# Performance work log

Hardware: AMD Instinct MI355X
Metric: run time of the kernel (lower is better)

The kernel has to match this reference:

```python
import jax, jax.numpy as jnp
import numpy as np

DIM = 1024
HEADS = 8
HEAD_DIM = DIM // HEADS
D_STATE = 256
BATCH = 8192
DT_MIN = 1e-3
DT_MAX = 1e-1
EPS = 1e-4  # RMSNorm eps


def setup_inputs() -> dict:
    key = jax.random.key(0)
    ks = jax.random.split(key, 8)
    x_t = jax.random.normal(ks[0], (BATCH, DIM), dtype=jnp.float32)
    state_re = jax.random.normal(ks[1], (BATCH, HEADS, D_STATE), dtype=jnp.float32)
    state_im = jax.random.normal(ks[2], (BATCH, HEADS, D_STATE), dtype=jnp.float32)
    # parameters (match torch init)
    norm_weight = jnp.ones((DIM,), dtype=jnp.float32)
    A_re_log = jnp.full((HEADS, D_STATE), float(np.log(0.5)), dtype=jnp.float32)
    n = jnp.arange(1, D_STATE + 1, dtype=jnp.float32)
    A_im = jnp.broadcast_to(float(np.pi) * n, (HEADS, D_STATE)).astype(jnp.float32)
    b_scale = 1.0 / float(np.sqrt(HEAD_DIM))
    c_scale = 1.0 / float(np.sqrt(D_STATE))
    B_re = jax.random.normal(ks[3], (HEADS, D_STATE, HEAD_DIM), dtype=jnp.float32) * b_scale
    B_im = jax.random.normal(ks[4], (HEADS, D_STATE, HEAD_DIM), dtype=jnp.float32) * b_scale
    C_re = jax.random.normal(ks[5], (HEADS, HEAD_DIM, D_STATE), dtype=jnp.float32) * c_scale
    C_im = jax.random.normal(ks[6], (HEADS, HEAD_DIM, D_STATE), dtype=jnp.float32) * c_scale
    D = jnp.ones((DIM,), dtype=jnp.float32)
    # log_dt: inverse-softplus of log-uniform dt in [dt_min, dt_max]
    u = jax.random.uniform(ks[7], (HEADS, D_STATE), dtype=jnp.float32)
    dt = jnp.exp(u * (np.log(DT_MAX) - np.log(DT_MIN)) + np.log(DT_MIN))
    dt = jnp.maximum(dt, 1e-4)
    log_dt = dt + jnp.log(-jnp.expm1(-dt))
    return dict(x_t=x_t, state_re=state_re, state_im=state_im,
                norm_weight=norm_weight, A_re_log=A_re_log, A_im=A_im,
                B_re=B_re, B_im=B_im, C_re=C_re, C_im=C_im, D=D, log_dt=log_dt)


def reference(x_t, state_re, state_im, norm_weight, A_re_log, A_im,
              B_re, B_im, C_re, C_im, D, log_dt):
    batch = x_t.shape[0]
    # RMSNorm (eps=1e-4, elementwise affine)
    ms = jnp.mean(jnp.square(x_t), axis=-1, keepdims=True)
    x = x_t * jax.lax.rsqrt(ms + EPS) * norm_weight
    x_h = x.reshape(batch, HEADS, HEAD_DIM)  # (B,H,P)
    # discretize
    A = jax.lax.complex(-jnp.exp(A_re_log), A_im)            # (H,N)
    dt = jax.nn.softplus(log_dt)                              # (H,N)
    A_bar = jnp.exp(dt.astype(A.dtype) * A)                   # (H,N) complex
    B = jax.lax.complex(B_re, B_im)                           # (H,N,P)
    C = jax.lax.complex(C_re, C_im)                           # (H,P,N)
    B_bar = ((A_bar - 1.0) / A)[..., None] * B                # (H,N,P)
    # recurrent step
    state = jax.lax.complex(state_re, state_im)               # (B,H,N)
    Bx = jnp.einsum('hnp,bhp->bhn', B_bar, x_h.astype(B_bar.dtype))
    new_state = A_bar[None] * state + Bx                      # (B,H,N)
    Ch = jnp.einsum('hpn,bhn->bhp', C, new_state)             # (B,H,P)
    D_h = D.reshape(HEADS, HEAD_DIM)[None]                    # (1,H,P)
    y_h = 2.0 * Ch.real + D_h * x_h
    out = x_t + y_h.reshape(batch, DIM)
    return out, new_state.real, new_state.imag
```

## Files before the change

kernel.cpp:

```cpp
#include <hip/hip_runtime.h>

#define BATCH 8192
#define DIM 1024
#define HEADS 8
#define HEAD_DIM 128
#define DSTATE 256

typedef __attribute__((ext_vector_type(8))) short short8v;
typedef __attribute__((ext_vector_type(4))) float f32x4;
typedef __attribute__((ext_vector_type(4))) unsigned short ushort4v;
typedef __attribute__((ext_vector_type(4))) unsigned int uint4v;

__device__ __forceinline__ unsigned short f2bf(float x) {
  unsigned int u = __builtin_bit_cast(unsigned int, x);
  unsigned int r = u + 0x7FFFu + ((u >> 16) & 1u);
  return (unsigned short)(r >> 16);
}
__device__ __forceinline__ float bf2f(unsigned short h) {
  unsigned int u = ((unsigned int)h) << 16;
  return __builtin_bit_cast(float, u);
}

__device__ __forceinline__ void stage16f(const float* g, float* l) {
  __builtin_amdgcn_global_load_lds(
      (const __attribute__((address_space(1))) unsigned int*)g,
      (__attribute__((address_space(3))) unsigned int*)l, 16, 0, 0);
}
__device__ __forceinline__ void stage4f(const float* g, float* l) {
  __builtin_amdgcn_global_load_lds(
      (const __attribute__((address_space(1))) unsigned int*)g,
      (__attribute__((address_space(3))) unsigned int*)l, 4, 0, 0);
}

#define BARRIER() do { \
  asm volatile("s_waitcnt lgkmcnt(0)" ::: "memory"); \
  __builtin_amdgcn_s_barrier(); \
  asm volatile("" ::: "memory"); } while (0)


__global__ __launch_bounds__(256) void prep(
    const float* __restrict__ logdt, const float* __restrict__ arelog,
    const float* __restrict__ aim,
    const float* __restrict__ Bre, const float* __restrict__ Bim,
    const float* __restrict__ Cre, const float* __restrict__ Cim,
    const float* __restrict__ xtg, const float* __restrict__ normw,
    unsigned short* __restrict__ w1re, unsigned short* __restrict__ w1im,
    unsigned short* __restrict__ w2re, unsigned short* __restrict__ w2mi,
    float* __restrict__ abr, float* __restrict__ abi,
    float* __restrict__ scale) {
  const int blk = blockIdx.x;
  if (blk < 1024) {
    const int i = blk * 256 + threadIdx.x;
    const int p = i & 127, s = (i >> 7) & 255, h = i >> 15;
    const int kk = s >> 4, u = s & 15;
    const int n = ((kk >> 1) << 5) + ((u >> 2) & 3) * 8 + (kk & 1) * 4 + (u & 3);
    const int hn = h * 256 + n;
    const float ld = logdt[hn];
    const float dt = log1pf(expf(ld));
    const float Ar = -expf(arelog[hn]);
    const float Ai = aim[hn];
    const float e = expf(dt * Ar), th = dt * Ai;
    const float Abr = e * cosf(th), Abi = e * sinf(th);
    if (p == 0) { abr[h * 256 + s] = Abr; abi[h * 256 + s] = Abi; }
    const float den = Ar * Ar + Ai * Ai;
    const float br_ = Abr - 1.0f;
    const float cr = (br_ * Ar + Abi * Ai) / den;
    const float ci = (Abi * Ar - br_ * Ai) / den;
    const int src = hn * 128 + p;
    const float wb = normw[h * 128 + p];
    const float bre = Bre[src], bim = Bim[src];
    w1re[i] = f2bf((cr * bre - ci * bim) * wb);
    w1im[i] = f2bf((cr * bim + ci * bre) * wb);
  } else if (blk < 2048) {
    const int i = (blk - 1024) * 256 + threadIdx.x;
    w2re[i] = f2bf(Cre[i]);
    w2mi[i] = f2bf(-Cim[i]);
  } else {
    const int wid = threadIdx.x >> 6, lane = threadIdx.x & 63;
    const int row = (blk - 2048) * 4 + wid;
    const float* xr = xtg + (size_t)row * DIM;
    float ssq = 0.f;
    #pragma unroll
    for (int c = 0; c < 4; ++c) {
      const f32x4 v = *(const f32x4*)(xr + c * 256 + lane * 4);
      ssq += v[0]*v[0] + v[1]*v[1] + v[2]*v[2] + v[3]*v[3];
    }
    #pragma unroll
    for (int m = 1; m < 64; m <<= 1) ssq += __shfl_xor(ssq, m, 64);
    if (lane == 0) scale[row] = rsqrtf(ssq * (1.0f / DIM) + 1e-4f);
  }
}

__global__ __launch_bounds__(512, 2) void s5_main(
    const unsigned short* __restrict__ w1re, const unsigned short* __restrict__ w1im,
    const unsigned short* __restrict__ w2re, const unsigned short* __restrict__ w2mi,
    const float* __restrict__ abrp, const float* __restrict__ abip,
    const float* __restrict__ scale,
    const float* __restrict__ sre, const float* __restrict__ sim,
    const float* __restrict__ xt, const float* __restrict__ dvec,
    const float* __restrict__ normw,
    float* __restrict__ out, float* __restrict__ nsre, float* __restrict__ nsim) {
  __shared__ float Sb[3][2][16][256];
  __shared__ float xtl[3][16][128];
  __shared__ unsigned short pf[2][8][64][8];
  __shared__ float scL[3][64];
  const int tid = threadIdx.x;
  const int w = tid >> 6, lane = tid & 63;
  const int g = lane >> 4, bl = lane & 15;
  const int h = blockIdx.x & 7;
  const int blkrow = (blockIdx.x >> 3) * 256;

  short8v w1r[2][4], w1i[2][4];
  #pragma unroll
  for (int t = 0; t < 2; ++t) {
    const int kk = 2 * w + t;
    const unsigned short* pr = w1re + ((size_t)(h * DSTATE + kk * 16 + bl)) * HEAD_DIM + g * 8;
    const unsigned short* pi = w1im + ((size_t)(h * DSTATE + kk * 16 + bl)) * HEAD_DIM + g * 8;
    #pragma unroll
    for (int ks = 0; ks < 4; ++ks) {
      w1r[t][ks] = *(const short8v*)(pr + ks * 32);
      w1i[t][ks] = *(const short8v*)(pi + ks * 32);
    }
  }
  short8v w2r[8], w2i[8];
  {
    const unsigned short* qr = w2re + ((size_t)(h * HEAD_DIM + w * 16 + bl)) * DSTATE + g * 8;
    const unsigned short* qi = w2mi + ((size_t)(h * HEAD_DIM + w * 16 + bl)) * DSTATE + g * 8;
    #pragma unroll
    for (int j = 0; j < 8; ++j) {
      w2r[j] = *(const short8v*)(qr + j * 32);
      w2i[j] = *(const short8v*)(qi + j * 32);
    }
  }
  f32x4 Arh[2], Aih[2];
  #pragma unroll
  for (int t = 0; t < 2; ++t) {
    Arh[t] = *(const f32x4*)(abrp + h * DSTATE + (2 * w + t) * 16 + g * 4);
    Aih[t] = *(const f32x4*)(abip + h * DSTATE + (2 * w + t) * 16 + g * 4);
  }
  f32x4 d4;
  {
    const int col = h * HEAD_DIM + w * 16 + g * 4;
    const f32x4 dv = *(const f32x4*)(dvec + col);
    const f32x4 nv = *(const f32x4*)(normw + col);
    #pragma unroll
    for (int r = 0; r < 4; ++r) d4[r] = dv[r] * nv[r];
  }

  auto STAGE = [&](int t, int b3) {
    const int gr0 = blkrow + t * 16;
    #pragma unroll
    for (int i = 0; i < 2; ++i) {
      const int row = 2 * w + i;
      const size_t rb = ((size_t)(gr0 + row) * HEADS + h) * DSTATE;
      const int soff = (lane ^ (row & 7)) * 4;
      stage16f(sre + rb + soff, &Sb[b3][0][row][0]);
      stage16f(sim + rb + soff, &Sb[b3][1][row][0]);
    }
    {
      const int row = 2 * w + (lane >> 5);
      const int soff = ((lane & 31) ^ (row & 7)) * 4;
      const float* src = xt + (size_t)(gr0 + row) * DIM + h * HEAD_DIM + soff;
      stage16f(src, &xtl[b3][2 * w][0]);
    }
    stage4f(scale + gr0 + (lane & 15), &scL[b3][0]);
  };

  STAGE(0, 0);
  STAGE(1, 1);

  for (int t = 0; t < 16; ++t) {
    const int bcur = t % 3;
    if (t < 2) { asm volatile("s_waitcnt vmcnt(6)"  ::: "memory"); }
    else       { asm volatile("s_waitcnt vmcnt(10)" ::: "memory"); }
    BARRIER();

    if (t + 2 < 16) STAGE(t + 2, (t + 2) % 3);

    const float scl = scL[bcur][bl];
    short8v xf[4];
    #pragma unroll
    for (int ks = 0; ks < 4; ++ks) {
      const f32x4 x0 = *(const f32x4*)&xtl[bcur][bl][(((ks * 8 + 2 * g)     ^ (bl & 7)) << 2)];
      const f32x4 x1 = *(const f32x4*)&xtl[bcur][bl][(((ks * 8 + 2 * g + 1) ^ (bl & 7)) << 2)];
      uint4v uv;
      uv[0] = (unsigned)f2bf(x0[0] * scl) | ((unsigned)f2bf(x0[1] * scl) << 16);
      uv[1] = (unsigned)f2bf(x0[2] * scl) | ((unsigned)f2bf(x0[3] * scl) << 16);
      uv[2] = (unsigned)f2bf(x1[0] * scl) | ((unsigned)f2bf(x1[1] * scl) << 16);
      uv[3] = (unsigned)f2bf(x1[2] * scl) | ((unsigned)f2bf(x1[3] * scl) << 16);
      xf[ks] = __builtin_bit_cast(short8v, uv);
    }

    unsigned pr0 = 0, pr1 = 0, pi0 = 0, pi1 = 0;
    #pragma unroll
    for (int tt = 0; tt < 2; ++tt) {
      f32x4 dr = {0.f,0.f,0.f,0.f};
      f32x4 di = {0.f,0.f,0.f,0.f};
      #pragma unroll
      for (int ks = 0; ks < 4; ++ks)
        dr = __builtin_amdgcn_mfma_f32_16x16x32_bf16(w1r[tt][ks], xf[ks], dr, 0, 0, 0);
      #pragma unroll
      for (int ks = 0; ks < 4; ++ks)
        di = __builtin_amdgcn_mfma_f32_16x16x32_bf16(w1i[tt][ks], xf[ks], di, 0, 0, 0);
      const int c = (((8 * w + 2 * g + tt) ^ (bl & 7)) << 2);
      const f32x4 s_r = *(const f32x4*)&Sb[bcur][0][bl][c];
      const f32x4 s_i = *(const f32x4*)&Sb[bcur][1][bl][c];
      f32x4 nr, ni;
      #pragma unroll
      for (int r = 0; r < 4; ++r) {
        nr[r] = fmaf(Arh[tt][r], s_r[r], fmaf(-Aih[tt][r], s_i[r], dr[r]));
        ni[r] = fmaf(Arh[tt][r], s_i[r], fmaf(Aih[tt][r], s_r[r], di[r]));
      }
      *(f32x4*)&Sb[bcur][0][bl][c] = nr;
      *(f32x4*)&Sb[bcur][1][bl][c] = ni;
      unsigned lo  = (unsigned)f2bf(nr[0]) | ((unsigned)f2bf(nr[1]) << 16);
      unsigned hi  = (unsigned)f2bf(nr[2]) | ((unsigned)f2bf(nr[3]) << 16);
      unsigned lo2 = (unsigned)f2bf(ni[0]) | ((unsigned)f2bf(ni[1]) << 16);
      unsigned hi2 = (unsigned)f2bf(ni[2]) | ((unsigned)f2bf(ni[3]) << 16);
      if (tt == 0) { pr0 = lo; pr1 = hi; pi0 = lo2; pi1 = hi2; }
      else {
        uint4v urv; urv[0] = pr0; urv[1] = pr1; urv[2] = lo;  urv[3] = hi;
        uint4v uiv; uiv[0] = pi0; uiv[1] = pi1; uiv[2] = lo2; uiv[3] = hi2;
        *(short8v*)&pf[0][w][lane][0] = __builtin_bit_cast(short8v, urv);
        *(short8v*)&pf[1][w][lane][0] = __builtin_bit_cast(short8v, uiv);
      }
    }
    BARRIER();

    #pragma unroll
    for (int i = 0; i < 2; ++i) {
      const int row = 2 * w + i;
      const size_t rb = ((size_t)(blkrow + t * 16 + row) * HEADS + h) * DSTATE;
      const int gc = (lane ^ (row & 7)) * 4;
      const f32x4 vr = *(const f32x4*)&Sb[bcur][0][row][lane * 4];
      const f32x4 vi = *(const f32x4*)&Sb[bcur][1][row][lane * 4];
      *(f32x4*)(nsre + rb + gc) = vr;
      *(f32x4*)(nsim + rb + gc) = vi;
    }

    f32x4 a2 = {0.f,0.f,0.f,0.f};
    #pragma unroll
    for (int j = 0; j < 8; ++j) {
      const short8v pbr = *(const short8v*)&pf[0][j][lane][0];
      const short8v pbi = *(const short8v*)&pf[1][j][lane][0];
      a2 = __builtin_amdgcn_mfma_f32_16x16x32_bf16(w2r[j], pbr, a2, 0, 0, 0);
      a2 = __builtin_amdgcn_mfma_f32_16x16x32_bf16(w2i[j], pbi, a2, 0, 0, 0);
    }

    {
      const int col = h * HEAD_DIM + w * 16 + g * 4;
      const size_t o = (size_t)(blkrow + t * 16 + bl) * DIM + col;
      const f32x4 xt4 = *(const f32x4*)&xtl[bcur][bl][(((4 * w + g) ^ (bl & 7)) << 2)];
      f32x4 ro;
      #pragma unroll
      for (int r = 0; r < 4; ++r)
        ro[r] = xt4[r] * (1.0f + d4[r] * scl) + 2.0f * a2[r];
      *(f32x4*)(out + o) = ro;
    }
  }
}

extern "C" void kernel_launch(void* const* d_in, const int* in_sizes, int n_in,
                              void* d_out, int out_size, void* d_ws, size_t ws_size,
                              hipStream_t stream) {
  const float* x_t      = (const float*)d_in[0];
  const float* state_re = (const float*)d_in[1];
  const float* state_im = (const float*)d_in[2];
  const float* norm_w   = (const float*)d_in[3];
  const float* A_re_log = (const float*)d_in[4];
  const float* A_im     = (const float*)d_in[5];
  const float* B_re     = (const float*)d_in[6];
  const float* B_im     = (const float*)d_in[7];
  const float* C_re     = (const float*)d_in[8];
  const float* C_im     = (const float*)d_in[9];
  const float* Dv       = (const float*)d_in[10];
  const float* log_dt   = (const float*)d_in[11];

  float* out   = (float*)d_out;
  float* ns_re = out + (size_t)BATCH * DIM;
  float* ns_im = ns_re + (size_t)BATCH * HEADS * DSTATE;

  char* ws = (char*)d_ws;
  unsigned short* w1re = (unsigned short*)ws;
  unsigned short* w1im = w1re + 262144;
  unsigned short* w2re = w1im + 262144;
  unsigned short* w2mi = w2re + 262144;
  float* abr   = (float*)(ws + 4 * 524288);
  float* abi   = abr + 2048;
  float* scale = abi + 2048;

  prep<<<4096, 256, 0, stream>>>(log_dt, A_re_log, A_im, B_re, B_im, C_re, C_im,
                                 x_t, norm_w, w1re, w1im, w2re, w2mi,
                                 abr, abi, scale);
  s5_main<<<256, 512, 0, stream>>>(w1re, w1im, w2re, w2mi, abr, abi, scale,
                                   state_re, state_im, x_t, Dv, norm_w,
                                   out, ns_re, ns_im);
}
```

Baseline: 92.30 us.

## Software-pipeline S5 phases, stage bf16 x_t, and drop the pf LDS buffer

The prep kernel now also writes a bf16 copy of x_t, and the main kernel stages that copy instead of fp32 x_t. The per-tile loop is restructured so the output phase of tile t-1 overlaps the state-update phase of tile t. This uses a 4-deep state ring and one barrier per iteration instead of two. The second MFMA reads the updated state straight from Sb instead of a separate packed pf buffer, and the output and state stores are made nontemporal. The risk is accuracy: the residual x_t added to out is now read back from bf16, and the prep kernel has extra writes.

```diff
diff --git a/kernel.cpp b/kernel.cpp
--- a/kernel.cpp
+++ b/kernel.cpp
@@ -26,7 +26,7 @@
       (const __attribute__((address_space(1))) unsigned int*)g,
       (__attribute__((address_space(3))) unsigned int*)l, 16, 0, 0);
 }
-__device__ __forceinline__ void stage4f(const float* g, float* l) {
+__device__ __forceinline__ void stage4u(const unsigned short* g, unsigned short* l) {
   __builtin_amdgcn_global_load_lds(
       (const __attribute__((address_space(1))) unsigned int*)g,
       (__attribute__((address_space(3))) unsigned int*)l, 4, 0, 0);
@@ -47,7 +47,7 @@
     unsigned short* __restrict__ w1re, unsigned short* __restrict__ w1im,
     unsigned short* __restrict__ w2re, unsigned short* __restrict__ w2mi,
     float* __restrict__ abr, float* __restrict__ abi,
-    float* __restrict__ scale) {
+    float* __restrict__ scale, unsigned short* __restrict__ xtb) {
   const int blk = blockIdx.x;
   if (blk < 1024) {
     const int i = blk * 256 + threadIdx.x;
@@ -79,11 +79,15 @@
     const int wid = threadIdx.x >> 6, lane = threadIdx.x & 63;
     const int row = (blk - 2048) * 4 + wid;
     const float* xr = xtg + (size_t)row * DIM;
+    unsigned short* xo = xtb + (size_t)row * DIM;
     float ssq = 0.f;
     #pragma unroll
     for (int c = 0; c < 4; ++c) {
       const f32x4 v = *(const f32x4*)(xr + c * 256 + lane * 4);
       ssq += v[0]*v[0] + v[1]*v[1] + v[2]*v[2] + v[3]*v[3];
+      ushort4v o;
+      o[0] = f2bf(v[0]); o[1] = f2bf(v[1]); o[2] = f2bf(v[2]); o[3] = f2bf(v[3]);
+      *(ushort4v*)(xo + c * 256 + lane * 4) = o;
     }
     #pragma unroll
     for (int m = 1; m < 64; m <<= 1) ssq += __shfl_xor(ssq, m, 64);
@@ -95,15 +99,13 @@
     const unsigned short* __restrict__ w1re, const unsigned short* __restrict__ w1im,
     const unsigned short* __restrict__ w2re, const unsigned short* __restrict__ w2mi,
     const float* __restrict__ abrp, const float* __restrict__ abip,
-    const float* __restrict__ scale,
+    const float* __restrict__ scale, const unsigned short* __restrict__ xtb,
     const float* __restrict__ sre, const float* __restrict__ sim,
-    const float* __restrict__ xt, const float* __restrict__ dvec,
-    const float* __restrict__ normw,
+    const float* __restrict__ dvec, const float* __restrict__ normw,
     float* __restrict__ out, float* __restrict__ nsre, float* __restrict__ nsim) {
-  __shared__ float Sb[3][2][16][256];
-  __shared__ float xtl[3][16][128];
-  __shared__ unsigned short pf[2][8][64][8];
-  __shared__ float scL[3][64];
+  __shared__ float Sb[4][2][16][256];
+  __shared__ unsigned short xbL[4][16][128];
+  __shared__ float scL[256];
   const int tid = threadIdx.x;
   const int w = tid >> 6, lane = tid & 63;
   const int g = lane >> 4, bl = lane & 15;
@@ -147,51 +149,42 @@
     for (int r = 0; r < 4; ++r) d4[r] = dv[r] * nv[r];
   }
 
-  auto STAGE = [&](int t, int b3) {
+  auto STAGE = [&](int t, int b) {
     const int gr0 = blkrow + t * 16;
     #pragma unroll
     for (int i = 0; i < 2; ++i) {
       const int row = 2 * w + i;
       const size_t rb = ((size_t)(gr0 + row) * HEADS + h) * DSTATE;
       const int soff = (lane ^ (row & 7)) * 4;
-      stage16f(sre + rb + soff, &Sb[b3][0][row][0]);
-      stage16f(sim + rb + soff, &Sb[b3][1][row][0]);
-    }
-    {
-      const int row = 2 * w + (lane >> 5);
-      const int soff = ((lane & 31) ^ (row & 7)) * 4;
-      const float* src = xt + (size_t)(gr0 + row) * DIM + h * HEAD_DIM + soff;
-      stage16f(src, &xtl[b3][2 * w][0]);
-    }
-    stage4f(scale + gr0 + (lane & 15), &scL[b3][0]);
+      stage16f(sre + rb + soff, &Sb[b][0][row][0]);
+      stage16f(sim + rb + soff, &Sb[b][1][row][0]);
+    }
+    #pragma unroll
+    for (int i = 0; i < 2; ++i) {
+      const int row = 2 * w + i;
+      const unsigned short* src = xtb + (size_t)(gr0 + row) * DIM + h * HEAD_DIM
+          + (((lane >> 2) ^ (row & 7)) << 3) + ((lane & 3) << 1);
+      stage4u(src, &xbL[b][row][0]);
+    }
   };
 
-  STAGE(0, 0);
-  STAGE(1, 1);
-
-  for (int t = 0; t < 16; ++t) {
-    const int bcur = t % 3;
-    if (t < 2) { asm volatile("s_waitcnt vmcnt(6)"  ::: "memory"); }
-    else       { asm volatile("s_waitcnt vmcnt(10)" ::: "memory"); }
-    BARRIER();
-
-    if (t + 2 < 16) STAGE(t + 2, (t + 2) % 3);
-
-    const float scl = scL[bcur][bl];
+  auto PHASE1 = [&](int t) {
+    const int b = t & 3;
+    const float scl = scL[t * 16 + bl];
     short8v xf[4];
     #pragma unroll
     for (int ks = 0; ks < 4; ++ks) {
-      const f32x4 x0 = *(const f32x4*)&xtl[bcur][bl][(((ks * 8 + 2 * g)     ^ (bl & 7)) << 2)];
-      const f32x4 x1 = *(const f32x4*)&xtl[bcur][bl][(((ks * 8 + 2 * g + 1) ^ (bl & 7)) << 2)];
-      uint4v uv;
-      uv[0] = (unsigned)f2bf(x0[0] * scl) | ((unsigned)f2bf(x0[1] * scl) << 16);
-      uv[1] = (unsigned)f2bf(x0[2] * scl) | ((unsigned)f2bf(x0[3] * scl) << 16);
-      uv[2] = (unsigned)f2bf(x1[0] * scl) | ((unsigned)f2bf(x1[1] * scl) << 16);
-      uv[3] = (unsigned)f2bf(x1[2] * scl) | ((unsigned)f2bf(x1[3] * scl) << 16);
-      xf[ks] = __builtin_bit_cast(short8v, uv);
-    }
-
-    unsigned pr0 = 0, pr1 = 0, pi0 = 0, pi1 = 0;
+      const int ch = (ks * 4 + g) ^ (bl & 7);
+      uint4v u = *(const uint4v*)&xbL[b][bl][ch * 8];
+      uint4v o;
+      #pragma unroll
+      for (int q = 0; q < 4; ++q) {
+        const float lo = bf2f((unsigned short)(u[q] & 0xffffu)) * scl;
+        const float hi = bf2f((unsigned short)(u[q] >> 16)) * scl;
+        o[q] = (unsigned)f2bf(lo) | ((unsigned)f2bf(hi) << 16);
+      }
+      xf[ks] = __builtin_bit_cast(short8v, o);
+    }
     #pragma unroll
     for (int tt = 0; tt < 2; ++tt) {
       f32x4 dr = {0.f,0.f,0.f,0.f};
@@ -203,61 +196,86 @@
       for (int ks = 0; ks < 4; ++ks)
         di = __builtin_amdgcn_mfma_f32_16x16x32_bf16(w1i[tt][ks], xf[ks], di, 0, 0, 0);
       const int c = (((8 * w + 2 * g + tt) ^ (bl & 7)) << 2);
-      const f32x4 s_r = *(const f32x4*)&Sb[bcur][0][bl][c];
-      const f32x4 s_i = *(const f32x4*)&Sb[bcur][1][bl][c];
+      const f32x4 s_r = *(const f32x4*)&Sb[b][0][bl][c];
+      const f32x4 s_i = *(const f32x4*)&Sb[b][1][bl][c];
       f32x4 nr, ni;
       #pragma unroll
       for (int r = 0; r < 4; ++r) {
         nr[r] = fmaf(Arh[tt][r], s_r[r], fmaf(-Aih[tt][r], s_i[r], dr[r]));
         ni[r] = fmaf(Arh[tt][r], s_i[r], fmaf(Aih[tt][r], s_r[r], di[r]));
       }
-      *(f32x4*)&Sb[bcur][0][bl][c] = nr;
-      *(f32x4*)&Sb[bcur][1][bl][c] = ni;
-      unsigned lo  = (unsigned)f2bf(nr[0]) | ((unsigned)f2bf(nr[1]) << 16);
-      unsigned hi  = (unsigned)f2bf(nr[2]) | ((unsigned)f2bf(nr[3]) << 16);
-      unsigned lo2 = (unsigned)f2bf(ni[0]) | ((unsigned)f2bf(ni[1]) << 16);
-      unsigned hi2 = (unsigned)f2bf(ni[2]) | ((unsigned)f2bf(ni[3]) << 16);
-      if (tt == 0) { pr0 = lo; pr1 = hi; pi0 = lo2; pi1 = hi2; }
-      else {
-        uint4v urv; urv[0] = pr0; urv[1] = pr1; urv[2] = lo;  urv[3] = hi;
-        uint4v uiv; uiv[0] = pi0; uiv[1] = pi1; uiv[2] = lo2; uiv[3] = hi2;
-        *(short8v*)&pf[0][w][lane][0] = __builtin_bit_cast(short8v, urv);
-        *(short8v*)&pf[1][w][lane][0] = __builtin_bit_cast(short8v, uiv);
-      }
-    }
-    BARRIER();
-
+      *(f32x4*)&Sb[b][0][bl][c] = nr;
+      *(f32x4*)&Sb[b][1][bl][c] = ni;
+    }
+  };
+
+  auto PHASE2 = [&](int t) {
+    const int b = t & 3;
     #pragma unroll
     for (int i = 0; i < 2; ++i) {
       const int row = 2 * w + i;
       const size_t rb = ((size_t)(blkrow + t * 16 + row) * HEADS + h) * DSTATE;
       const int gc = (lane ^ (row & 7)) * 4;
-      const f32x4 vr = *(const f32x4*)&Sb[bcur][0][row][lane * 4];
-      const f32x4 vi = *(const f32x4*)&Sb[bcur][1][row][lane * 4];
-      *(f32x4*)(nsre + rb + gc) = vr;
-      *(f32x4*)(nsim + rb + gc) = vi;
-    }
-
+      const f32x4 vr = *(const f32x4*)&Sb[b][0][row][lane * 4];
+      const f32x4 vi = *(const f32x4*)&Sb[b][1][row][lane * 4];
+      __builtin_nontemporal_store(vr, (f32x4*)(nsre + rb + gc));
+      __builtin_nontemporal_store(vi, (f32x4*)(nsim + rb + gc));
+    }
     f32x4 a2 = {0.f,0.f,0.f,0.f};
     #pragma unroll
     for (int j = 0; j < 8; ++j) {
-      const short8v pbr = *(const short8v*)&pf[0][j][lane][0];
-      const short8v pbi = *(const short8v*)&pf[1][j][lane][0];
+      const int c0 = (((8 * j + 2 * g)     ^ (bl & 7)) << 2);
+      const int c1 = (((8 * j + 2 * g + 1) ^ (bl & 7)) << 2);
+      const f32x4 r0 = *(const f32x4*)&Sb[b][0][bl][c0];
+      const f32x4 r1 = *(const f32x4*)&Sb[b][0][bl][c1];
+      const f32x4 i0 = *(const f32x4*)&Sb[b][1][bl][c0];
+      const f32x4 i1 = *(const f32x4*)&Sb[b][1][bl][c1];
+      uint4v ur, ui;
+      ur[0] = (unsigned)f2bf(r0[0]) | ((unsigned)f2bf(r0[1]) << 16);
+      ur[1] = (unsigned)f2bf(r0[2]) | ((unsigned)f2bf(r0[3]) << 16);
+      ur[2] = (unsigned)f2bf(r1[0]) | ((unsigned)f2bf(r1[1]) << 16);
+      ur[3] = (unsigned)f2bf(r1[2]) | ((unsigned)f2bf(r1[3]) << 16);
+      ui[0] = (unsigned)f2bf(i0[0]) | ((unsigned)f2bf(i0[1]) << 16);
+      ui[1] = (unsigned)f2bf(i0[2]) | ((unsigned)f2bf(i0[3]) << 16);
+      ui[2] = (unsigned)f2bf(i1[0]) | ((unsigned)f2bf(i1[1]) << 16);
+      ui[3] = (unsigned)f2bf(i1[2]) | ((unsigned)f2bf(i1[3]) << 16);
+      const short8v pbr = __builtin_bit_cast(short8v, ur);
+      const short8v pbi = __builtin_bit_cast(short8v, ui);
       a2 = __builtin_amdgcn_mfma_f32_16x16x32_bf16(w2r[j], pbr, a2, 0, 0, 0);
       a2 = __builtin_amdgcn_mfma_f32_16x16x32_bf16(w2i[j], pbi, a2, 0, 0, 0);
     }
-
-    {
-      const int col = h * HEAD_DIM + w * 16 + g * 4;
-      const size_t o = (size_t)(blkrow + t * 16 + bl) * DIM + col;
-      const f32x4 xt4 = *(const f32x4*)&xtl[bcur][bl][(((4 * w + g) ^ (bl & 7)) << 2)];
-      f32x4 ro;
-      #pragma unroll
-      for (int r = 0; r < 4; ++r)
-        ro[r] = xt4[r] * (1.0f + d4[r] * scl) + 2.0f * a2[r];
-      *(f32x4*)(out + o) = ro;
-    }
-  }
+    const float scl = scL[t * 16 + bl];
+    const int col = h * HEAD_DIM + w * 16 + g * 4;
+    const size_t o = (size_t)(blkrow + t * 16 + bl) * DIM + col;
+    const unsigned short* xp =
+        &xbL[b][bl][((((2 * w) + (g >> 1)) ^ (bl & 7)) << 3) + ((g & 1) << 2)];
+    f32x4 ro;
+    #pragma unroll
+    for (int r = 0; r < 4; ++r) {
+      const float xr = bf2f(xp[r]);
+      ro[r] = xr * (1.0f + d4[r] * scl) + 2.0f * a2[r];
+    }
+    __builtin_nontemporal_store(ro, (f32x4*)(out + o));
+  };
+
+  if (w == 0) stage16f(scale + blkrow + lane * 4, &scL[0]);
+  STAGE(0, 0);
+  STAGE(1, 1);
+  asm volatile("s_waitcnt vmcnt(6)" ::: "memory");
+
+  for (int t = 0; t < 16; ++t) {
+    if (t == 1)                asm volatile("s_waitcnt vmcnt(6)"  ::: "memory");
+    else if (t == 2)           asm volatile("s_waitcnt vmcnt(11)" ::: "memory");
+    else if (t >= 3 && t <= 14) asm volatile("s_waitcnt vmcnt(16)" ::: "memory");
+    else if (t == 15)          asm volatile("s_waitcnt vmcnt(10)" ::: "memory");
+    BARRIER();
+    if (t + 2 < 16) STAGE(t + 2, (t + 2) & 3);
+    __builtin_amdgcn_sched_barrier(0);
+    if (t > 0) PHASE2(t - 1);
+    PHASE1(t);
+  }
+  BARRIER();
+  PHASE2(15);
 }
 
 extern "C" void kernel_launch(void* const* d_in, const int* in_sizes, int n_in,
@@ -288,11 +306,12 @@
   float* abr   = (float*)(ws + 4 * 524288);
   float* abi   = abr + 2048;
   float* scale = abi + 2048;
+  unsigned short* xtb = (unsigned short*)(scale + 8192);
 
   prep<<<4096, 256, 0, stream>>>(log_dt, A_re_log, A_im, B_re, B_im, C_re, C_im,
                                  x_t, norm_w, w1re, w1im, w2re, w2mi,
-                                 abr, abi, scale);
-  s5_main<<<256, 512, 0, stream>>>(w1re, w1im, w2re, w2mi, abr, abi, scale,
-                                   state_re, state_im, x_t, Dv, norm_w,
+                                 abr, abi, scale, xtb);
+  s5_main<<<256, 512, 0, stream>>>(w1re, w1im, w2re, w2mi, abr, abi, scale, xtb,
+                                   state_re, state_im, Dv, norm_w,
                                    out, ns_re, ns_im);
 }
```

Result: slower. 96.21 us (+4.2%).

## Precompute bf16 normalized x and split main kernel across 16 waves

Applied to the files above, without the earlier changes.

The prep kernel now writes the RMS-normalized input as bf16 plus the inverse scale. The main kernel then stages bf16 x instead of fp32 and no longer converts it per tile. The main kernel doubles to 1024 threads: each wave owns one 16-state slice in phase 1. Phase 2 splits the output GEMM across two K-halves with an LDS reduction, and the output epilogue is deferred one iteration to overlap with the next tile. The residual is rebuilt from bf16 normalized x times the inverse scale, which lowers the precision of the out term and adds an extra bf16 write in prep.

```diff
diff --git a/kernel.cpp b/kernel.cpp
--- a/kernel.cpp
+++ b/kernel.cpp
@@ -10,6 +10,7 @@
 typedef __attribute__((ext_vector_type(4))) float f32x4;
 typedef __attribute__((ext_vector_type(4))) unsigned short ushort4v;
 typedef __attribute__((ext_vector_type(4))) unsigned int uint4v;
+typedef __attribute__((ext_vector_type(2))) unsigned int uint2v;
 
 __device__ __forceinline__ unsigned short f2bf(float x) {
   unsigned int u = __builtin_bit_cast(unsigned int, x);
@@ -26,7 +27,7 @@
       (const __attribute__((address_space(1))) unsigned int*)g,
       (__attribute__((address_space(3))) unsigned int*)l, 16, 0, 0);
 }
-__device__ __forceinline__ void stage4f(const float* g, float* l) {
+__device__ __forceinline__ void stage4u(const unsigned short* g, unsigned short* l) {
   __builtin_amdgcn_global_load_lds(
       (const __attribute__((address_space(1))) unsigned int*)g,
       (__attribute__((address_space(3))) unsigned int*)l, 4, 0, 0);
@@ -47,7 +48,7 @@
     unsigned short* __restrict__ w1re, unsigned short* __restrict__ w1im,
     unsigned short* __restrict__ w2re, unsigned short* __restrict__ w2mi,
     float* __restrict__ abr, float* __restrict__ abi,
-    float* __restrict__ scale) {
+    float* __restrict__ rscale, unsigned short* __restrict__ xhb) {
   const int blk = blockIdx.x;
   if (blk < 1024) {
     const int i = blk * 256 + threadIdx.x;
@@ -79,185 +80,187 @@
     const int wid = threadIdx.x >> 6, lane = threadIdx.x & 63;
     const int row = (blk - 2048) * 4 + wid;
     const float* xr = xtg + (size_t)row * DIM;
+    unsigned short* xo = xhb + (size_t)row * DIM;
+    f32x4 v[4];
     float ssq = 0.f;
     #pragma unroll
     for (int c = 0; c < 4; ++c) {
-      const f32x4 v = *(const f32x4*)(xr + c * 256 + lane * 4);
-      ssq += v[0]*v[0] + v[1]*v[1] + v[2]*v[2] + v[3]*v[3];
+      v[c] = *(const f32x4*)(xr + c * 256 + lane * 4);
+      ssq += v[c][0]*v[c][0] + v[c][1]*v[c][1] + v[c][2]*v[c][2] + v[c][3]*v[c][3];
     }
     #pragma unroll
     for (int m = 1; m < 64; m <<= 1) ssq += __shfl_xor(ssq, m, 64);
-    if (lane == 0) scale[row] = rsqrtf(ssq * (1.0f / DIM) + 1e-4f);
-  }
-}
-
-__global__ __launch_bounds__(512, 2) void s5_main(
+    const float sc = rsqrtf(ssq * (1.0f / DIM) + 1e-4f);
+    if (lane == 0) rscale[row] = 1.0f / sc;
+    #pragma unroll
+    for (int c = 0; c < 4; ++c) {
+      ushort4v o;
+      o[0] = f2bf(v[c][0] * sc); o[1] = f2bf(v[c][1] * sc);
+      o[2] = f2bf(v[c][2] * sc); o[3] = f2bf(v[c][3] * sc);
+      *(ushort4v*)(xo + c * 256 + lane * 4) = o;
+    }
+  }
+}
+
+__global__ __launch_bounds__(1024, 4) void s5_main(
     const unsigned short* __restrict__ w1re, const unsigned short* __restrict__ w1im,
     const unsigned short* __restrict__ w2re, const unsigned short* __restrict__ w2mi,
     const float* __restrict__ abrp, const float* __restrict__ abip,
-    const float* __restrict__ scale,
+    const float* __restrict__ rscale, const unsigned short* __restrict__ xhb,
     const float* __restrict__ sre, const float* __restrict__ sim,
-    const float* __restrict__ xt, const float* __restrict__ dvec,
-    const float* __restrict__ normw,
+    const float* __restrict__ dvec, const float* __restrict__ normw,
     float* __restrict__ out, float* __restrict__ nsre, float* __restrict__ nsim) {
   __shared__ float Sb[3][2][16][256];
-  __shared__ float xtl[3][16][128];
+  __shared__ unsigned short xbL[4][16][128];
   __shared__ unsigned short pf[2][8][64][8];
-  __shared__ float scL[3][64];
+  __shared__ float red[8][64][4];
+  __shared__ float rsL[256];
   const int tid = threadIdx.x;
   const int w = tid >> 6, lane = tid & 63;
   const int g = lane >> 4, bl = lane & 15;
   const int h = blockIdx.x & 7;
   const int blkrow = (blockIdx.x >> 3) * 256;
-
-  short8v w1r[2][4], w1i[2][4];
-  #pragma unroll
-  for (int t = 0; t < 2; ++t) {
-    const int kk = 2 * w + t;
-    const unsigned short* pr = w1re + ((size_t)(h * DSTATE + kk * 16 + bl)) * HEAD_DIM + g * 8;
-    const unsigned short* pi = w1im + ((size_t)(h * DSTATE + kk * 16 + bl)) * HEAD_DIM + g * 8;
+  const int j = w >> 1, tt = w & 1;
+  const int pt = w >> 1, kh = w & 1;
+
+  short8v w1r[4], w1i[4];
+  {
+    const unsigned short* pr = w1re + ((size_t)(h * DSTATE + w * 16 + bl)) * HEAD_DIM + g * 8;
+    const unsigned short* pi = w1im + ((size_t)(h * DSTATE + w * 16 + bl)) * HEAD_DIM + g * 8;
     #pragma unroll
     for (int ks = 0; ks < 4; ++ks) {
-      w1r[t][ks] = *(const short8v*)(pr + ks * 32);
-      w1i[t][ks] = *(const short8v*)(pi + ks * 32);
-    }
-  }
-  short8v w2r[8], w2i[8];
+      w1r[ks] = *(const short8v*)(pr + ks * 32);
+      w1i[ks] = *(const short8v*)(pi + ks * 32);
+    }
+  }
+  short8v w2r[4], w2i[4];
   {
-    const unsigned short* qr = w2re + ((size_t)(h * HEAD_DIM + w * 16 + bl)) * DSTATE + g * 8;
-    const unsigned short* qi = w2mi + ((size_t)(h * HEAD_DIM + w * 16 + bl)) * DSTATE + g * 8;
-    #pragma unroll
-    for (int j = 0; j < 8; ++j) {
-      w2r[j] = *(const short8v*)(qr + j * 32);
-      w2i[j] = *(const short8v*)(qi + j * 32);
-    }
-  }
-  f32x4 Arh[2], Aih[2];
-  #pragma unroll
-  for (int t = 0; t < 2; ++t) {
-    Arh[t] = *(const f32x4*)(abrp + h * DSTATE + (2 * w + t) * 16 + g * 4);
-    Aih[t] = *(const f32x4*)(abip + h * DSTATE + (2 * w + t) * 16 + g * 4);
-  }
+    const unsigned short* qr = w2re + ((size_t)(h * HEAD_DIM + pt * 16 + bl)) * DSTATE + kh * 128 + g * 8;
+    const unsigned short* qi = w2mi + ((size_t)(h * HEAD_DIM + pt * 16 + bl)) * DSTATE + kh * 128 + g * 8;
+    #pragma unroll
+    for (int jj = 0; jj < 4; ++jj) {
+      w2r[jj] = *(const short8v*)(qr + jj * 32);
+      w2i[jj] = *(const short8v*)(qi + jj * 32);
+    }
+  }
+  const f32x4 Arh = *(const f32x4*)(abrp + h * DSTATE + w * 16 + g * 4);
+  const f32x4 Aih = *(const f32x4*)(abip + h * DSTATE + w * 16 + g * 4);
   f32x4 d4;
   {
-    const int col = h * HEAD_DIM + w * 16 + g * 4;
+    const int col = h * HEAD_DIM + pt * 16 + g * 4;
     const f32x4 dv = *(const f32x4*)(dvec + col);
     const f32x4 nv = *(const f32x4*)(normw + col);
     #pragma unroll
     for (int r = 0; r < 4; ++r) d4[r] = dv[r] * nv[r];
   }
-
-  auto STAGE = [&](int t, int b3) {
+  f32x4 savedA2 = {0.f, 0.f, 0.f, 0.f};
+
+  auto STAGE = [&](int t) {
+    const int b3 = t % 3, b4 = t & 3;
     const int gr0 = blkrow + t * 16;
-    #pragma unroll
-    for (int i = 0; i < 2; ++i) {
-      const int row = 2 * w + i;
-      const size_t rb = ((size_t)(gr0 + row) * HEADS + h) * DSTATE;
-      const int soff = (lane ^ (row & 7)) * 4;
-      stage16f(sre + rb + soff, &Sb[b3][0][row][0]);
-      stage16f(sim + rb + soff, &Sb[b3][1][row][0]);
-    }
-    {
-      const int row = 2 * w + (lane >> 5);
-      const int soff = ((lane & 31) ^ (row & 7)) * 4;
-      const float* src = xt + (size_t)(gr0 + row) * DIM + h * HEAD_DIM + soff;
-      stage16f(src, &xtl[b3][2 * w][0]);
-    }
-    stage4f(scale + gr0 + (lane & 15), &scL[b3][0]);
+    const size_t rb = ((size_t)(gr0 + w) * HEADS + h) * DSTATE;
+    const int soff = (lane ^ (w & 7)) * 4;
+    stage16f(sre + rb + soff, &Sb[b3][0][w][0]);
+    stage16f(sim + rb + soff, &Sb[b3][1][w][0]);
+    const unsigned short* xs = xhb + (size_t)(gr0 + w) * DIM + h * HEAD_DIM
+        + (((lane >> 2) ^ (w & 7)) << 3) + ((lane & 3) << 1);
+    stage4u(xs, &xbL[b4][w][0]);
   };
 
-  STAGE(0, 0);
-  STAGE(1, 1);
+  auto PHASE1 = [&](int t) {
+    const int b3 = t % 3, b4 = t & 3;
+    short8v xf[4];
+    #pragma unroll
+    for (int ks = 0; ks < 4; ++ks)
+      xf[ks] = *(const short8v*)&xbL[b4][bl][(((ks * 4 + g) ^ (bl & 7)) << 3)];
+    f32x4 dr = {0.f,0.f,0.f,0.f};
+    f32x4 di = {0.f,0.f,0.f,0.f};
+    #pragma unroll
+    for (int ks = 0; ks < 4; ++ks)
+      dr = __builtin_amdgcn_mfma_f32_16x16x32_bf16(w1r[ks], xf[ks], dr, 0, 0, 0);
+    #pragma unroll
+    for (int ks = 0; ks < 4; ++ks)
+      di = __builtin_amdgcn_mfma_f32_16x16x32_bf16(w1i[ks], xf[ks], di, 0, 0, 0);
+    const int c = (((8 * j + 2 * g + tt) ^ (bl & 7)) << 2);
+    const f32x4 s_r = *(const f32x4*)&Sb[b3][0][bl][c];
+    const f32x4 s_i = *(const f32x4*)&Sb[b3][1][bl][c];
+    f32x4 nr, ni;
+    #pragma unroll
+    for (int r = 0; r < 4; ++r) {
+      nr[r] = fmaf(Arh[r], s_r[r], fmaf(-Aih[r], s_i[r], dr[r]));
+      ni[r] = fmaf(Arh[r], s_i[r], fmaf(Aih[r], s_r[r], di[r]));
+    }
+    *(f32x4*)&Sb[b3][0][bl][c] = nr;
+    *(f32x4*)&Sb[b3][1][bl][c] = ni;
+    uint2v ur, ui;
+    ur[0] = (unsigned)f2bf(nr[0]) | ((unsigned)f2bf(nr[1]) << 16);
+    ur[1] = (unsigned)f2bf(nr[2]) | ((unsigned)f2bf(nr[3]) << 16);
+    ui[0] = (unsigned)f2bf(ni[0]) | ((unsigned)f2bf(ni[1]) << 16);
+    ui[1] = (unsigned)f2bf(ni[2]) | ((unsigned)f2bf(ni[3]) << 16);
+    *(uint2v*)&pf[0][j][lane][tt * 4] = ur;
+    *(uint2v*)&pf[1][j][lane][tt * 4] = ui;
+  };
+
+  auto PHASE2 = [&](int t) {
+    const int b3 = t % 3;
+    const size_t rb = ((size_t)(blkrow + t * 16 + w) * HEADS + h) * DSTATE;
+    const int gc = (lane ^ (w & 7)) * 4;
+    const f32x4 vr = *(const f32x4*)&Sb[b3][0][w][lane * 4];
+    const f32x4 vi = *(const f32x4*)&Sb[b3][1][w][lane * 4];
+    *(f32x4*)(nsre + rb + gc) = vr;
+    *(f32x4*)(nsim + rb + gc) = vi;
+    f32x4 a2 = {0.f,0.f,0.f,0.f};
+    #pragma unroll
+    for (int jj = 0; jj < 4; ++jj) {
+      const short8v pbr = *(const short8v*)&pf[0][kh * 4 + jj][lane][0];
+      const short8v pbi = *(const short8v*)&pf[1][kh * 4 + jj][lane][0];
+      a2 = __builtin_amdgcn_mfma_f32_16x16x32_bf16(w2r[jj], pbr, a2, 0, 0, 0);
+      a2 = __builtin_amdgcn_mfma_f32_16x16x32_bf16(w2i[jj], pbi, a2, 0, 0, 0);
+    }
+    if (kh) *(f32x4*)&red[pt][lane][0] = a2;
+    else savedA2 = a2;
+  };
+
+  auto EPILOG = [&](int tm) {
+    const f32x4 p = *(const f32x4*)&red[pt][lane][0];
+    const float rs = rsL[tm * 16 + bl];
+    const unsigned short* xp =
+        &xbL[tm & 3][bl][(((2 * pt + (g >> 1)) ^ (bl & 7)) << 3) + ((g & 1) << 2)];
+    f32x4 ro;
+    #pragma unroll
+    for (int r = 0; r < 4; ++r)
+      ro[r] = bf2f(xp[r]) * (rs + d4[r]) + 2.0f * (savedA2[r] + p[r]);
+    const size_t o = (size_t)(blkrow + tm * 16 + bl) * DIM + h * HEAD_DIM + pt * 16 + g * 4;
+    *(f32x4*)(out + o) = ro;
+  };
+
+  if (w == 0) stage16f(rscale + blkrow + lane * 4, &rsL[0]);
+  STAGE(0);
+  STAGE(1);
 
   for (int t = 0; t < 16; ++t) {
-    const int bcur = t % 3;
-    if (t < 2) { asm volatile("s_waitcnt vmcnt(6)"  ::: "memory"); }
-    else       { asm volatile("s_waitcnt vmcnt(10)" ::: "memory"); }
+    if (t == 0)      asm volatile("s_waitcnt vmcnt(3)" ::: "memory");
+    else if (t == 1) asm volatile("s_waitcnt vmcnt(5)" ::: "memory");
+    else if (t == 2) {
+      if (kh == 0) asm volatile("s_waitcnt vmcnt(8)" ::: "memory");
+      else         asm volatile("s_waitcnt vmcnt(7)" ::: "memory");
+    } else if (t <= 14) {
+      if (kh == 0) asm volatile("s_waitcnt vmcnt(9)" ::: "memory");
+      else         asm volatile("s_waitcnt vmcnt(7)" ::: "memory");
+    } else {
+      if (kh == 0) asm volatile("s_waitcnt vmcnt(6)" ::: "memory");
+      else         asm volatile("s_waitcnt vmcnt(4)" ::: "memory");
+    }
     BARRIER();
-
-    if (t + 2 < 16) STAGE(t + 2, (t + 2) % 3);
-
-    const float scl = scL[bcur][bl];
-    short8v xf[4];
-    #pragma unroll
-    for (int ks = 0; ks < 4; ++ks) {
-      const f32x4 x0 = *(const f32x4*)&xtl[bcur][bl][(((ks * 8 + 2 * g)     ^ (bl & 7)) << 2)];
-      const f32x4 x1 = *(const f32x4*)&xtl[bcur][bl][(((ks * 8 + 2 * g + 1) ^ (bl & 7)) << 2)];
-      uint4v uv;
-      uv[0] = (unsigned)f2bf(x0[0] * scl) | ((unsigned)f2bf(x0[1] * scl) << 16);
-      uv[1] = (unsigned)f2bf(x0[2] * scl) | ((unsigned)f2bf(x0[3] * scl) << 16);
-      uv[2] = (unsigned)f2bf(x1[0] * scl) | ((unsigned)f2bf(x1[1] * scl) << 16);
-      uv[3] = (unsigned)f2bf(x1[2] * scl) | ((unsigned)f2bf(x1[3] * scl) << 16);
-      xf[ks] = __builtin_bit_cast(short8v, uv);
-    }
-
-    unsigned pr0 = 0, pr1 = 0, pi0 = 0, pi1 = 0;
-    #pragma unroll
-    for (int tt = 0; tt < 2; ++tt) {
-      f32x4 dr = {0.f,0.f,0.f,0.f};
-      f32x4 di = {0.f,0.f,0.f,0.f};
-      #pragma unroll
-      for (int ks = 0; ks < 4; ++ks)
-        dr = __builtin_amdgcn_mfma_f32_16x16x32_bf16(w1r[tt][ks], xf[ks], dr, 0, 0, 0);
-      #pragma unroll
-      for (int ks = 0; ks < 4; ++ks)
-        di = __builtin_amdgcn_mfma_f32_16x16x32_bf16(w1i[tt][ks], xf[ks], di, 0, 0, 0);
-      const int c = (((8 * w + 2 * g + tt) ^ (bl & 7)) << 2);
-      const f32x4 s_r = *(const f32x4*)&Sb[bcur][0][bl][c];
-      const f32x4 s_i = *(const f32x4*)&Sb[bcur][1][bl][c];
-      f32x4 nr, ni;
-      #pragma unroll
-      for (int r = 0; r < 4; ++r) {
-        nr[r] = fmaf(Arh[tt][r], s_r[r], fmaf(-Aih[tt][r], s_i[r], dr[r]));
-        ni[r] = fmaf(Arh[tt][r], s_i[r], fmaf(Aih[tt][r], s_r[r], di[r]));
-      }
-      *(f32x4*)&Sb[bcur][0][bl][c] = nr;
-      *(f32x4*)&Sb[bcur][1][bl][c] = ni;
-      unsigned lo  = (unsigned)f2bf(nr[0]) | ((unsigned)f2bf(nr[1]) << 16);
-      unsigned hi  = (unsigned)f2bf(nr[2]) | ((unsigned)f2bf(nr[3]) << 16);
-      unsigned lo2 = (unsigned)f2bf(ni[0]) | ((unsigned)f2bf(ni[1]) << 16);
-      unsigned hi2 = (unsigned)f2bf(ni[2]) | ((unsigned)f2bf(ni[3]) << 16);
-      if (tt == 0) { pr0 = lo; pr1 = hi; pi0 = lo2; pi1 = hi2; }
-      else {
-        uint4v urv; urv[0] = pr0; urv[1] = pr1; urv[2] = lo;  urv[3] = hi;
-        uint4v uiv; uiv[0] = pi0; uiv[1] = pi1; uiv[2] = lo2; uiv[3] = hi2;
-        *(short8v*)&pf[0][w][lane][0] = __builtin_bit_cast(short8v, urv);
-        *(short8v*)&pf[1][w][lane][0] = __builtin_bit_cast(short8v, uiv);
-      }
-    }
+    if (t + 2 < 16) STAGE(t + 2);
+    __builtin_amdgcn_sched_barrier(0);
+    if (t > 0 && kh == 0) EPILOG(t - 1);
+    PHASE1(t);
     BARRIER();
-
-    #pragma unroll
-    for (int i = 0; i < 2; ++i) {
-      const int row = 2 * w + i;
-      const size_t rb = ((size_t)(blkrow + t * 16 + row) * HEADS + h) * DSTATE;
-      const int gc = (lane ^ (row & 7)) * 4;
-      const f32x4 vr = *(const f32x4*)&Sb[bcur][0][row][lane * 4];
-      const f32x4 vi = *(const f32x4*)&Sb[bcur][1][row][lane * 4];
-      *(f32x4*)(nsre + rb + gc) = vr;
-      *(f32x4*)(nsim + rb + gc) = vi;
-    }
-
-    f32x4 a2 = {0.f,0.f,0.f,0.f};
-    #pragma unroll
-    for (int j = 0; j < 8; ++j) {
-      const short8v pbr = *(const short8v*)&pf[0][j][lane][0];
-      const short8v pbi = *(const short8v*)&pf[1][j][lane][0];
-      a2 = __builtin_amdgcn_mfma_f32_16x16x32_bf16(w2r[j], pbr, a2, 0, 0, 0);
-      a2 = __builtin_amdgcn_mfma_f32_16x16x32_bf16(w2i[j], pbi, a2, 0, 0, 0);
-    }
-
-    {
-      const int col = h * HEAD_DIM + w * 16 + g * 4;
-      const size_t o = (size_t)(blkrow + t * 16 + bl) * DIM + col;
-      const f32x4 xt4 = *(const f32x4*)&xtl[bcur][bl][(((4 * w + g) ^ (bl & 7)) << 2)];
-      f32x4 ro;
-      #pragma unroll
-      for (int r = 0; r < 4; ++r)
-        ro[r] = xt4[r] * (1.0f + d4[r] * scl) + 2.0f * a2[r];
-      *(f32x4*)(out + o) = ro;
-    }
-  }
+    PHASE2(t);
+  }
+  BARRIER();
+  if (kh == 0) EPILOG(15);
 }
 
 extern "C" void kernel_launch(void* const* d_in, const int* in_sizes, int n_in,
@@ -285,14 +288,15 @@
   unsigned short* w1im = w1re + 262144;
   unsigned short* w2re = w1im + 262144;
   unsigned short* w2mi = w2re + 262144;
-  float* abr   = (float*)(ws + 4 * 524288);
-  float* abi   = abr + 2048;
-  float* scale = abi + 2048;
+  float* abr    = (float*)(ws + 4 * 524288);
+  float* abi    = abr + 2048;
+  float* rscale = abi + 2048;
+  unsigned short* xhb = (unsigned short*)(rscale + 8192);
 
   prep<<<4096, 256, 0, stream>>>(log_dt, A_re_log, A_im, B_re, B_im, C_re, C_im,
                                  x_t, norm_w, w1re, w1im, w2re, w2mi,
-                                 abr, abi, scale);
-  s5_main<<<256, 512, 0, stream>>>(w1re, w1im, w2re, w2mi, abr, abi, scale,
-                                   state_re, state_im, x_t, Dv, norm_w,
-                                   out, ns_re, ns_im);
-}
+                                 abr, abi, rscale, xhb);
+  s5_main<<<256, 1024, 0, stream>>>(w1re, w1im, w2re, w2mi, abr, abi, rscale, xhb,
+                                    state_re, state_im, Dv, norm_w,
+                                    out, ns_re, ns_im);
+}
```

New measurement: 107.7 us. +16.7%, slower.
